# Optimization experiments

Hardware: AMD Instinct MI355X
Metric: run time of the kernel (lower is better)

The kernel has to match this reference:

```python
import jax, jax.numpy as jnp
import numpy as np

N_EMBD, N_HEAD, HEAD_DIM = 1024, 16, 64
N_EXPERTS, TOP_K, EXPERT_DIM = 8, 2, 2048
EPS = 1e-5


def rmsnorm(x):
    return x * jax.lax.rsqrt(jnp.mean(x * x, axis=-1, keepdims=True) + EPS)


def setup_inputs() -> dict:
    key = jax.random.key(0)
    ks = jax.random.split(key, 9)
    s = 0.02
    x = jax.random.normal(ks[0], (2, 2048, N_EMBD), dtype=jnp.float32)
    # weights stored [in, out] (torch Linear applies x @ W.T; we pre-transpose)
    wq = jax.random.normal(ks[1], (N_EMBD, N_EMBD), dtype=jnp.float32) * s
    wk = jax.random.normal(ks[2], (N_EMBD, N_EMBD), dtype=jnp.float32) * s
    wv = jax.random.normal(ks[3], (N_EMBD, N_EMBD), dtype=jnp.float32) * s
    wo = jax.random.normal(ks[4], (N_EMBD, N_EMBD), dtype=jnp.float32) * s
    router_w = jax.random.normal(ks[5], (N_EMBD, N_EXPERTS), dtype=jnp.float32) * s
    exp_fc1 = jax.random.normal(ks[6], (N_EXPERTS, N_EMBD, EXPERT_DIM), dtype=jnp.float32) * s
    exp_fc2 = jax.random.normal(ks[7], (N_EXPERTS, EXPERT_DIM, N_EMBD), dtype=jnp.float32) * s
    return {"x": x, "wq": wq, "wk": wk, "wv": wv, "wo": wo,
            "router_w": router_w, "exp_fc1": exp_fc1, "exp_fc2": exp_fc2}


def _attn(h, wq, wk, wv, wo):
    B, T, C = h.shape
    sc = 1.0 / np.sqrt(HEAD_DIM)
    q = (h @ wq).reshape(B, T, N_HEAD, HEAD_DIM)
    k = (h @ wk).reshape(B, T, N_HEAD, HEAD_DIM)
    v = (h @ wv).reshape(B, T, N_HEAD, HEAD_DIM)
    s = jnp.einsum('bqhd,bkhd->bhqk', q, k) * sc
    causal = jnp.triu(jnp.ones((T, T), dtype=bool), 1)
    s = jnp.where(causal, -jnp.inf, s)
    a = jax.nn.softmax(s, axis=-1)
    o = jnp.einsum('bhqk,bkhd->bqhd', a, v).reshape(B, T, C)
    return o @ wo


def _moe(h, router_w, exp_fc1, exp_fc2):
    B, T, D = h.shape
    xf = h.reshape(B * T, D)
    probs = jax.nn.softmax(xf @ router_w, axis=-1)          # [N, E]
    top_vals, top_idx = jax.lax.top_k(probs, TOP_K)          # [N, K]
    top_vals = top_vals / jnp.sum(top_vals, axis=-1, keepdims=True)
    # combine weight per (token, expert); top_k indices are distinct
    combine = jnp.sum(jax.nn.one_hot(top_idx, N_EXPERTS, dtype=xf.dtype)
                      * top_vals[..., None], axis=1)         # [N, E]
    h1 = jnp.square(jax.nn.relu(jnp.einsum('nd,edh->neh', xf, exp_fc1)))
    oe = jnp.einsum('neh,ehd->ned', h1, exp_fc2)             # [N, E, D]
    out = jnp.einsum('ned,ne->nd', oe, combine)
    return out.reshape(B, T, D)


def reference(x, wq, wk, wv, wo, router_w, exp_fc1, exp_fc2):
    x = x + _attn(rmsnorm(x), wq, wk, wv, wo)
    x = x + _moe(rmsnorm(x), router_w, exp_fc1, exp_fc2)
    return x
```

## Files before the change

kernel.cpp:

```cpp
#include <hip/hip_runtime.h>
#include <math.h>

#define NTOK 4096
#define DEMB 1024
#define TSEQ 2048
#define QKVS 3072
#define QKN  2048
#define EDIM 2048
#define NEXP 8

typedef unsigned short u16;
typedef unsigned int u32;
typedef __bf16 bf16_t;
typedef __bf16 bf16x8 __attribute__((ext_vector_type(8)));
typedef __bf16 bf16x4 __attribute__((ext_vector_type(4)));
typedef float f32x4 __attribute__((ext_vector_type(4)));

__device__ __forceinline__ f32x4 mfma16(bf16x8 a, bf16x8 b, f32x4 c) {
    return __builtin_amdgcn_mfma_f32_16x16x32_bf16(a, b, c, 0, 0, 0);
}
__device__ __forceinline__ void gll16(const void* g, void* l) {
    __builtin_amdgcn_global_load_lds((const __attribute__((address_space(1))) u32*)g,
                                     (__attribute__((address_space(3))) u32*)l, 16, 0, 0);
}
__device__ __forceinline__ u16 f2bf(float x) {
    union { __bf16 h; u16 u; } c; c.h = (__bf16)x; return c.u;
}

__global__ __launch_bounds__(256) void rmsnorm_split_k(const float* __restrict__ x,
                                                       bf16_t* __restrict__ hi,
                                                       bf16_t* __restrict__ lo) {
    const int row = blockIdx.x;
    const float4 v = ((const float4*)(x + (size_t)row * DEMB))[threadIdx.x];
    float ss = v.x*v.x + v.y*v.y + v.z*v.z + v.w*v.w;
    #pragma unroll
    for (int off = 32; off; off >>= 1) ss += __shfl_xor(ss, off);
    __shared__ float wsum[4];
    if ((threadIdx.x & 63) == 0) wsum[threadIdx.x >> 6] = ss;
    __syncthreads();
    const float r = rsqrtf((wsum[0]+wsum[1]+wsum[2]+wsum[3]) * (1.0f/DEMB) + 1e-5f);
    const float f[4] = {v.x*r, v.y*r, v.z*r, v.w*r};
    bf16x4 hv, lv;
    #pragma unroll
    for (int j = 0; j < 4; j++) {
        const __bf16 hb = (__bf16)f[j];
        hv[j] = hb;
        lv[j] = (__bf16)(f[j] - (float)hb);
    }
    ((bf16x4*)(hi + (size_t)row*DEMB))[threadIdx.x] = hv;
    ((bf16x4*)(lo + (size_t)row*DEMB))[threadIdx.x] = lv;
}

__global__ __launch_bounds__(256) void rmsnorm_bf_k(const float* __restrict__ x,
                                                    bf16_t* __restrict__ y) {
    const int row = blockIdx.x;
    const float4 v = ((const float4*)(x + (size_t)row * DEMB))[threadIdx.x];
    float ss = v.x*v.x + v.y*v.y + v.z*v.z + v.w*v.w;
    #pragma unroll
    for (int off = 32; off; off >>= 1) ss += __shfl_xor(ss, off);
    __shared__ float wsum[4];
    if ((threadIdx.x & 63) == 0) wsum[threadIdx.x >> 6] = ss;
    __syncthreads();
    const float r = rsqrtf((wsum[0]+wsum[1]+wsum[2]+wsum[3]) * (1.0f/DEMB) + 1e-5f);
    bf16x4 o;
    o[0] = (__bf16)(v.x*r); o[1] = (__bf16)(v.y*r);
    o[2] = (__bf16)(v.z*r); o[3] = (__bf16)(v.w*r);
    ((bf16x4*)(y + (size_t)row*DEMB))[threadIdx.x] = o;
}

__global__ __launch_bounds__(256) void transp_split_k(const float* __restrict__ w,
                                                      bf16_t* __restrict__ wth,
                                                      bf16_t* __restrict__ wtl,
                                                      int K, int M) {
    __shared__ float t[32][33];
    const int m0 = blockIdx.x*32, k0 = blockIdx.y*32;
    const int tx = threadIdx.x & 31, ty = threadIdx.x >> 5;
    #pragma unroll
    for (int i = 0; i < 32; i += 8) t[ty+i][tx] = w[(size_t)(k0+ty+i)*M + m0+tx];
    __syncthreads();
    #pragma unroll
    for (int i = 0; i < 32; i += 8) {
        const float f = t[tx][ty+i];
        const __bf16 hb = (__bf16)f;
        wth[(size_t)(m0+ty+i)*K + k0+tx] = hb;
        wtl[(size_t)(m0+ty+i)*K + k0+tx] = (__bf16)(f - (float)hb);
    }
}

__global__ __launch_bounds__(256) void transp_k(const float* __restrict__ w,
                                                bf16_t* __restrict__ wt,
                                                int K, int M) {
    __shared__ float t[32][33];
    const size_t eo = (size_t)blockIdx.z * K * M;
    w += eo; wt += eo;
    const int m0 = blockIdx.x*32, k0 = blockIdx.y*32;
    const int tx = threadIdx.x & 31, ty = threadIdx.x >> 5;
    #pragma unroll
    for (int i = 0; i < 32; i += 8) t[ty+i][tx] = w[(size_t)(k0+ty+i)*M + m0+tx];
    __syncthreads();
    #pragma unroll
    for (int i = 0; i < 32; i += 8) wt[(size_t)(m0+ty+i)*K + k0+tx] = (__bf16)t[tx][ty+i];
}

template<int EPI>
__global__ __launch_bounds__(256) void gemm_split(const bf16_t* __restrict__ Ah,
                                                  const bf16_t* __restrict__ Al,
                                                  const bf16_t* __restrict__ Bh,
                                                  const bf16_t* __restrict__ Bl,
                                                  const float* __restrict__ res,
                                                  float* __restrict__ C,
                                                  bf16_t* __restrict__ qkh,
                                                  bf16_t* __restrict__ qkl,
                                                  bf16_t* __restrict__ vth,
                                                  bf16_t* __restrict__ vtl,
                                                  int N, int K) {
    __shared__ u16 As[16384];
    __shared__ u16 Bs[16384];
    const int tid = threadIdx.x;
    const int lane = tid & 63, w = tid >> 6;
    const int lr = lane & 15, lg = lane >> 4;
    const int wm = w >> 1, wn = w & 1;
    const int nbx = gridDim.x;
    const int nwg = gridDim.x * gridDim.y;
    int flat = blockIdx.y * nbx + blockIdx.x;
    flat = (flat & 7) * (nwg >> 3) + (flat >> 3);
    const int m0 = (flat / nbx) * 128, n0 = (flat % nbx) * 128;

    const int srow = tid >> 3;
    const int sd   = (tid & 7) ^ (srow & 7);
    const int kofs = (sd & 3) * 8;
    const bf16_t* Asrc = (sd < 4) ? Ah : Al;
    const bf16_t* Bsrc = (sd < 4) ? Bh : Bl;
    const bf16_t* pa0 = Asrc + (size_t)(m0 + srow     ) * K + kofs;
    const bf16_t* pa1 = Asrc + (size_t)(m0 + srow + 32) * K + kofs;
    const bf16_t* pa2 = Asrc + (size_t)(m0 + srow + 64) * K + kofs;
    const bf16_t* pa3 = Asrc + (size_t)(m0 + srow + 96) * K + kofs;
    const bf16_t* pb0 = Bsrc + (size_t)(n0 + srow     ) * K + kofs;
    const bf16_t* pb1 = Bsrc + (size_t)(n0 + srow + 32) * K + kofs;
    const bf16_t* pb2 = Bsrc + (size_t)(n0 + srow + 64) * K + kofs;
    const bf16_t* pb3 = Bsrc + (size_t)(n0 + srow + 96) * K + kofs;
    char* dA = (char*)As + tid*16;
    char* dB = (char*)Bs + tid*16;
    const int ca = (lg ^ (lr & 7)) * 8;

    auto STG = [&](int bsel, int kk) {
        char* a_ = dA + bsel*16384;
        char* b_ = dB + bsel*16384;
        gll16(pa0 + kk, a_);          gll16(pa1 + kk, a_ + 4096);
        gll16(pa2 + kk, a_ + 8192);   gll16(pa3 + kk, a_ + 12288);
        gll16(pb0 + kk, b_);          gll16(pb1 + kk, b_ + 4096);
        gll16(pb2 + kk, b_ + 8192);   gll16(pb3 + kk, b_ + 12288);
    };

    STG(0, 0);
    asm volatile("s_waitcnt vmcnt(0)" ::: "memory");
    __syncthreads();
    f32x4 acc[4][4] = {};
    int cur = 0;
    for (int k0 = 0; k0 < K; k0 += 32) {
        if (k0 + 32 < K) STG(cur ^ 1, k0 + 32);
        const u16* Ab = As + cur*8192;
        const u16* Bb = Bs + cur*8192;
        bf16x8 ah[4], al[4], bh[4], bl[4];
        #pragma unroll
        for (int i = 0; i < 4; i++) {
            const int ao = (wm*64 + i*16 + lr)*64 + ca;
            const int bo = (wn*64 + i*16 + lr)*64 + ca;
            ah[i] = *(const bf16x8*)&Ab[ao];
            al[i] = *(const bf16x8*)&Ab[ao ^ 32];
            bh[i] = *(const bf16x8*)&Bb[bo];
            bl[i] = *(const bf16x8*)&Bb[bo ^ 32];
        }
        #pragma unroll
        for (int i = 0; i < 4; i++)
            #pragma unroll
            for (int j = 0; j < 4; j++) {
                acc[i][j] = mfma16(ah[i], bh[j], acc[i][j]);
                acc[i][j] = mfma16(ah[i], bl[j], acc[i][j]);
                acc[i][j] = mfma16(al[i], bh[j], acc[i][j]);
            }
        asm volatile("s_waitcnt vmcnt(0)" ::: "memory");
        __syncthreads();
        cur ^= 1;
    }
    #pragma unroll
    for (int i = 0; i < 4; i++) {
        #pragma unroll
        for (int j = 0; j < 4; j++) {
            const int row = m0 + wm*64 + i*16 + lg*4;
            const int col = n0 + wn*64 + j*16 + lr;
            const f32x4 v = acc[i][j];
            if (EPI == 1) {
                #pragma unroll
                for (int r = 0; r < 4; r++) {
                    const size_t o = (size_t)(row + r) * N + col;
                    C[o] = res[o] + v[r];
                }
            } else {
                if (col < QKN) {
                    const float sc = (col < DEMB) ? 0.125f : 1.0f;
                    #pragma unroll
                    for (int r = 0; r < 4; r++) {
                        const size_t o = (size_t)(row + r) * QKN + col;
                        const float f = v[r] * sc;
                        const __bf16 hb = (__bf16)f;
                        qkh[o] = hb;
                        qkl[o] = (__bf16)(f - (float)hb);
                    }
                } else {
                    const int d = col - QKN;
                    const int hh = d >> 6, dd = d & 63;
                    const int bb = row >> 11, t = row & 2047;
                    const size_t base = ((size_t)(bb*16 + hh)*64 + dd) * TSEQ + t;
                    #pragma unroll
                    for (int r = 0; r < 4; r++) {
                        const float f = v[r];
                        const __bf16 hb = (__bf16)f;
                        vth[base + r] = hb;
                        vtl[base + r] = (__bf16)(f - (float)hb);
                    }
                }
            }
        }
    }
}

template<int EPI, int GATHER>
__global__ __launch_bounds__(256) void gemm_moe(const bf16_t* __restrict__ A,
                                                const bf16_t* __restrict__ Ball,
                                                bf16_t* __restrict__ C,
                                                const int* __restrict__ rowmap,
                                                const int* __restrict__ counts,
                                                const int* __restrict__ offs,
                                                int N, int K) {
    const int e = blockIdx.z;
    const int cnt = counts[e];
    if ((int)blockIdx.y * 128 >= cnt) return;
    const int base = offs[e];
    const bf16_t* Bt = Ball + (size_t)e * N * K;
    __shared__ u16 As[8192];
    __shared__ u16 Bs[8192];
    const int tid = threadIdx.x;
    const int lane = tid & 63, w = tid >> 6;
    const int lr = lane & 15, lg = lane >> 4;
    const int wm = w >> 1, wn = w & 1;
    const int m0 = blockIdx.y * 128, n0 = blockIdx.x * 128;

    const int srp = tid >> 3;
    const int sd  = (tid & 7) ^ (srp & 7);
    const int smrow = 2*srp + (sd >> 2);
    const int kofs  = (sd & 3) * 8;
    const int l0 = min(m0 + smrow, cnt - 1), l1 = min(m0 + 64 + smrow, cnt - 1);
    const size_t r0 = GATHER ? (size_t)rowmap[base + l0] : (size_t)(base + l0);
    const size_t r1 = GATHER ? (size_t)rowmap[base + l1] : (size_t)(base + l1);
    const bf16_t* pa0 = A + r0 * K + kofs;
    const bf16_t* pa1 = A + r1 * K + kofs;
    const bf16_t* pb0 = Bt + (size_t)(n0 + smrow)      * K + kofs;
    const bf16_t* pb1 = Bt + (size_t)(n0 + 64 + smrow) * K + kofs;
    char* dA = (char*)As + tid*16;
    char* dB = (char*)Bs + tid*16;
    const int cs = (((lr & 1) << 2) + lg) ^ ((lr >> 1) & 7);

    auto STG = [&](int bsel, int kk) {
        char* a_ = dA + bsel*8192;
        char* b_ = dB + bsel*8192;
        gll16(pa0 + kk, a_); gll16(pa1 + kk, a_ + 4096);
        gll16(pb0 + kk, b_); gll16(pb1 + kk, b_ + 4096);
    };

    STG(0, 0);
    asm volatile("s_waitcnt vmcnt(0)" ::: "memory");
    __syncthreads();
    f32x4 acc[4][4] = {};
    int cur = 0;
    for (int k0 = 0; k0 < K; k0 += 32) {
        if (k0 + 32 < K) STG(cur ^ 1, k0 + 32);
        const u16* Ab = As + cur*4096;
        const u16* Bb = Bs + cur*4096;
        bf16x8 af[4], bfr[4];
        #pragma unroll
        for (int i = 0; i < 4; i++) {
            af[i]  = *(const bf16x8*)&Ab[(wm*32 + i*8 + (lr>>1))*64 + cs*8];
            bfr[i] = *(const bf16x8*)&Bb[(wn*32 + i*8 + (lr>>1))*64 + cs*8];
        }
        #pragma unroll
        for (int i = 0; i < 4; i++)
            #pragma unroll
            for (int j = 0; j < 4; j++)
                acc[i][j] = mfma16(af[i], bfr[j], acc[i][j]);
        asm volatile("s_waitcnt vmcnt(0)" ::: "memory");
        __syncthreads();
        cur ^= 1;
    }
    #pragma unroll
    for (int i = 0; i < 4; i++) {
        #pragma unroll
        for (int j = 0; j < 4; j++) {
            const int rowl = m0 + wm*64 + i*16 + lg*4;
            const int col  = n0 + wn*64 + j*16 + lr;
            const f32x4 v = acc[i][j];
            #pragma unroll
            for (int r = 0; r < 4; r++) {
                if (rowl + r < cnt) {
                    float xv = v[r];
                    if (EPI == 2) { xv = fmaxf(xv, 0.f); xv = xv * xv; }
                    C[(size_t)(base + rowl + r) * N + col] = (__bf16)xv;
                }
            }
        }
    }
}

__global__ __launch_bounds__(256) void attn_mfma(const bf16_t* __restrict__ qkh,
                                                 const bf16_t* __restrict__ qkl,
                                                 const bf16_t* __restrict__ vth,
                                                 const bf16_t* __restrict__ vtl,
                                                 bf16_t* __restrict__ aoh,
                                                 bf16_t* __restrict__ aol) {
    __shared__ u16 KsH[64*64];
    __shared__ u16 KsL[64*64];
    __shared__ u16 VtH[64*64];
    __shared__ u16 VtL[64*64];
    __shared__ u16 P_H[4*16*72];
    __shared__ u16 P_L[4*16*72];
    const int tid = threadIdx.x, lane = tid & 63, wv = tid >> 6;
    const int lr = lane & 15, lg = lane >> 4;
    const int L = blockIdx.x + blockIdx.y*16 + blockIdx.z*256;
    const int swz = (L & 7)*64 + (L >> 3);
    const int qa = swz & 15;
    const int h  = (swz >> 4) & 15;
    const int b  = swz >> 8;
    const int qb = 31 - qa;
    u16* plwH = P_H + wv * 16 * 72;
    u16* plwL = P_L + wv * 16 * 72;
    const int wq0A = qa*64 + wv*16;
    const int wq0B = qb*64 + wv*16;

    bf16x8 qAh[2], qAl[2], qBh[2], qBl[2];
    #pragma unroll
    for (int kf = 0; kf < 2; kf++) {
        const size_t qoA = (size_t)(b*TSEQ + wq0A + lr)*QKN + h*64 + kf*32 + lg*8;
        const size_t qoB = (size_t)(b*TSEQ + wq0B + lr)*QKN + h*64 + kf*32 + lg*8;
        qAh[kf] = *(const bf16x8*)(qkh + qoA);
        qAl[kf] = *(const bf16x8*)(qkl + qoA);
        qBh[kf] = *(const bf16x8*)(qkh + qoB);
        qBl[kf] = *(const bf16x8*)(qkl + qoB);
    }

    f32x4 ofA[4] = {}, ofB[4] = {};
    float mA = -1e30f, lA = 0.f, mB = -1e30f, lB = 0.f;

    const int skv = tid >> 3;
    const int pst = tid & 7;
    const int chs = pst ^ (skv & 7);
    const int bh = b*16 + h;
    const bf16_t* kh = qkh + 1024;
    const bf16_t* kl = qkl + 1024;
    const size_t vrow0 = (size_t)(bh*64 + skv)      * TSEQ;
    const size_t vrow1 = (size_t)(bh*64 + skv + 32) * TSEQ;

    auto step = [&](f32x4 (&of)[4], float& mrun, float& lrun,
                    const bf16x8 (&qfh)[2], const bf16x8 (&qfl)[2],
                    const int wq0, const bool diag, const int kvb) {
        f32x4 sf[4] = {};
        #pragma unroll
        for (int kf = 0; kf < 2; kf++)
            #pragma unroll
            for (int f = 0; f < 4; f++) {
                const int idx = (f*16 + lr)*64 + ((kf*32 + lg*8) ^ ((lr & 7) << 3));
                const bf16x8 ah = *(const bf16x8*)&KsH[idx];
                const bf16x8 al = *(const bf16x8*)&KsL[idx];
                sf[f] = mfma16(ah, qfh[kf], sf[f]);
                sf[f] = mfma16(ah, qfl[kf], sf[f]);
                sf[f] = mfma16(al, qfh[kf], sf[f]);
            }
        if (diag) {
            #pragma unroll
            for (int f = 0; f < 4; f++)
                #pragma unroll
                for (int r = 0; r < 4; r++)
                    if (kvb + f*16 + lg*4 + r > wq0 + lr) sf[f][r] = -1e30f;
        }
        float tm = -1e30f;
        #pragma unroll
        for (int f = 0; f < 4; f++)
            tm = fmaxf(tm, fmaxf(fmaxf(sf[f][0], sf[f][1]), fmaxf(sf[f][2], sf[f][3])));
        tm = fmaxf(tm, __shfl_xor(tm, 16));
        tm = fmaxf(tm, __shfl_xor(tm, 32));
        const float mnew = fmaxf(mrun, tm);
        const float fac = __expf(mrun - mnew);
        mrun = mnew;
        float ps = 0.f;
        #pragma unroll
        for (int f = 0; f < 4; f++) {
            float p[4];
            #pragma unroll
            for (int r = 0; r < 4; r++) { p[r] = __expf(sf[f][r] - mnew); ps += p[r]; }
            u16 hb4[4], lb4[4];
            #pragma unroll
            for (int r = 0; r < 4; r++) {
                const __bf16 hb = (__bf16)p[r];
                hb4[r] = f2bf(p[r]);
                lb4[r] = f2bf(p[r] - (float)hb);
            }
            u32* pwh = (u32*)&plwH[lr*72 + f*16 + lg*4];
            u32* pwl = (u32*)&plwL[lr*72 + f*16 + lg*4];
            pwh[0] = (u32)hb4[0] | ((u32)hb4[1] << 16);
            pwh[1] = (u32)hb4[2] | ((u32)hb4[3] << 16);
            pwl[0] = (u32)lb4[0] | ((u32)lb4[1] << 16);
            pwl[1] = (u32)lb4[2] | ((u32)lb4[3] << 16);
        }
        ps += __shfl_xor(ps, 16);
        ps += __shfl_xor(ps, 32);
        lrun = lrun*fac + ps;
        #pragma unroll
        for (int f2 = 0; f2 < 4; f2++)
            #pragma unroll
            for (int r = 0; r < 4; r++) of[f2][r] *= fac;
        #pragma unroll
        for (int hf = 0; hf < 2; hf++) {
            const bf16x8 pbh = *(const bf16x8*)&plwH[lr*72 + hf*32 + lg*8];
            const bf16x8 pbl = *(const bf16x8*)&plwL[lr*72 + hf*32 + lg*8];
            #pragma unroll
            for (int f2 = 0; f2 < 4; f2++) {
                const int vidx = (f2*16 + lr)*64 + (((hf*4 + lg) ^ (lr & 7)) << 3);
                const bf16x8 vah = *(const bf16x8*)&VtH[vidx];
                const bf16x8 val = *(const bf16x8*)&VtL[vidx];
                of[f2] = mfma16(vah, pbh, of[f2]);
                of[f2] = mfma16(vah, pbl, of[f2]);
                of[f2] = mfma16(val, pbh, of[f2]);
            }
        }
    };

    for (int kt = 0; kt <= qb; kt++) {
        __syncthreads();
        const size_t krow = (size_t)(b*TSEQ + kt*64 + skv)*QKN + h*64;
        gll16(kh + krow + chs*8,                     (char*)KsH + tid*16);
        gll16(kh + krow + (size_t)32*QKN + chs*8,    (char*)KsH + 4096 + tid*16);
        gll16(kl + krow + chs*8,                     (char*)KsL + tid*16);
        gll16(kl + krow + (size_t)32*QKN + chs*8,    (char*)KsL + 4096 + tid*16);
        gll16(vth + vrow0 + kt*64 + chs*8,           (char*)VtH + tid*16);
        gll16(vth + vrow1 + kt*64 + chs*8,           (char*)VtH + 4096 + tid*16);
        gll16(vtl + vrow0 + kt*64 + chs*8,           (char*)VtL + tid*16);
        gll16(vtl + vrow1 + kt*64 + chs*8,           (char*)VtL + 4096 + tid*16);
        __syncthreads();
        if (kt <= qa) step(ofA, mA, lA, qAh, qAl, wq0A, kt == qa, kt*64);
        step(ofB, mB, lB, qBh, qBl, wq0B, kt == qb, kt*64);
    }

    const float invA = 1.f / lA, invB = 1.f / lB;
    #pragma unroll
    for (int f2 = 0; f2 < 4; f2++) {
        u16 hb4[4], lb4[4];
        #pragma unroll
        for (int r = 0; r < 4; r++) {
            const float f = ofA[f2][r] * invA;
            const __bf16 hb = (__bf16)f;
            hb4[r] = f2bf(f);
            lb4[r] = f2bf(f - (float)hb);
        }
        u32* pwh = (u32*)&plwH[lr*72 + f2*16 + lg*4];
        u32* pwl = (u32*)&plwL[lr*72 + f2*16 + lg*4];
        pwh[0] = (u32)hb4[0] | ((u32)hb4[1] << 16);
        pwh[1] = (u32)hb4[2] | ((u32)hb4[3] << 16);
        pwl[0] = (u32)lb4[0] | ((u32)lb4[1] << 16);
        pwl[1] = (u32)lb4[2] | ((u32)lb4[3] << 16);
    }
    asm volatile("s_waitcnt lgkmcnt(0)" ::: "memory");
    __builtin_amdgcn_sched_barrier(0);
    #pragma unroll
    for (int pass = 0; pass < 2; pass++) {
        const int qlr = pass*8 + (lane >> 3);
        const int ch = (lane & 7) * 8;
        const bf16x8 oh = *(const bf16x8*)&plwH[qlr*72 + ch];
        const bf16x8 ol = *(const bf16x8*)&plwL[qlr*72 + ch];
        const size_t go = (size_t)(b*TSEQ + wq0A + qlr) * DEMB + h*64 + ch;
        *(bf16x8*)(aoh + go) = oh;
        *(bf16x8*)(aol + go) = ol;
    }
    asm volatile("s_waitcnt lgkmcnt(0)" ::: "memory");
    __builtin_amdgcn_sched_barrier(0);
    #pragma unroll
    for (int f2 = 0; f2 < 4; f2++) {
        u16 hb4[4], lb4[4];
        #pragma unroll
        for (int r = 0; r < 4; r++) {
            const float f = ofB[f2][r] * invB;
            const __bf16 hb = (__bf16)f;
            hb4[r] = f2bf(f);
            lb4[r] = f2bf(f - (float)hb);
        }
        u32* pwh = (u32*)&plwH[lr*72 + f2*16 + lg*4];
        u32* pwl = (u32*)&plwL[lr*72 + f2*16 + lg*4];
        pwh[0] = (u32)hb4[0] | ((u32)hb4[1] << 16);
        pwh[1] = (u32)hb4[2] | ((u32)hb4[3] << 16);
        pwl[0] = (u32)lb4[0] | ((u32)lb4[1] << 16);
        pwl[1] = (u32)lb4[2] | ((u32)lb4[3] << 16);
    }
    asm volatile("s_waitcnt lgkmcnt(0)" ::: "memory");
    __builtin_amdgcn_sched_barrier(0);
    #pragma unroll
    for (int pass = 0; pass < 2; pass++) {
        const int qlr = pass*8 + (lane >> 3);
        const int ch = (lane & 7) * 8;
        const bf16x8 oh = *(const bf16x8*)&plwH[qlr*72 + ch];
        const bf16x8 ol = *(const bf16x8*)&plwL[qlr*72 + ch];
        const size_t go = (size_t)(b*TSEQ + wq0B + qlr) * DEMB + h*64 + ch;
        *(bf16x8*)(aoh + go) = oh;
        *(bf16x8*)(aol + go) = ol;
    }
}

__global__ void zero8(int* c) { if (threadIdx.x < NEXP) c[threadIdx.x] = 0; }

__global__ __launch_bounds__(256) void router_k(const float* __restrict__ xout,
                                                const float* __restrict__ rw,
                                                int* __restrict__ idx,
                                                float* __restrict__ wts,
                                                int* __restrict__ pos,
                                                int* __restrict__ counts) {
    const int tok = blockIdx.x * 4 + (threadIdx.x >> 6);
    const int lane = threadIdx.x & 63;
    const float* xr = xout + (size_t)tok * DEMB;
    float ss = 0.f;
    float acc[NEXP];
    #pragma unroll
    for (int e = 0; e < NEXP; e++) acc[e] = 0.f;
    for (int kk = lane; kk < DEMB; kk += 64) {
        const float xv = xr[kk];
        ss += xv * xv;
        #pragma unroll
        for (int e = 0; e < NEXP; e++) acc[e] += xv * rw[kk*NEXP + e];
    }
    #pragma unroll
    for (int off = 32; off; off >>= 1) ss += __shfl_xor(ss, off);
    #pragma unroll
    for (int e = 0; e < NEXP; e++) {
        #pragma unroll
        for (int off = 32; off; off >>= 1) acc[e] += __shfl_xor(acc[e], off);
    }
    if (lane == 0) {
        const float r = rsqrtf(ss * (1.0f/DEMB) + 1e-5f);
        float v[NEXP];
        #pragma unroll
        for (int e = 0; e < NEXP; e++) v[e] = acc[e] * r;
        int b0 = 0; float v0 = v[0];
        #pragma unroll
        for (int e = 1; e < NEXP; e++) if (v[e] > v0) { v0 = v[e]; b0 = e; }
        int b1 = -1; float v1 = -1e30f;
        #pragma unroll
        for (int e = 0; e < NEXP; e++) if (e != b0 && v[e] > v1) { v1 = v[e]; b1 = e; }
        const float w0 = 1.f / (1.f + __expf(v1 - v0));
        idx[tok*2+0] = b0; idx[tok*2+1] = b1;
        wts[tok*2+0] = w0; wts[tok*2+1] = 1.f - w0;
        pos[tok*2+0] = atomicAdd(&counts[b0], 1);
        pos[tok*2+1] = atomicAdd(&counts[b1], 1);
    }
}

__global__ void offsets_k(const int* __restrict__ counts, int* __restrict__ offs) {
    if (threadIdx.x == 0) {
        int s = 0;
        for (int e = 0; e < NEXP; e++) { offs[e] = s; s += counts[e]; }
    }
}

__global__ __launch_bounds__(256) void buildmap_k(const int* __restrict__ idx,
                                                  const int* __restrict__ pos,
                                                  const int* __restrict__ offs,
                                                  int* __restrict__ rowmap,
                                                  int* __restrict__ rowpos) {
    const int n = blockIdx.x * 256 + threadIdx.x;
    #pragma unroll
    for (int s = 0; s < 2; s++) {
        const int e = idx[n*2+s];
        const int r = offs[e] + pos[n*2+s];
        rowmap[r] = n;
        rowpos[n*2+s] = r;
    }
}

__global__ __launch_bounds__(256) void combine_k(const bf16_t* __restrict__ oe,
                                                 const int* __restrict__ rowpos,
                                                 const float* __restrict__ wts,
                                                 float* __restrict__ out) {
    const int n = blockIdx.x;
    const int r0 = rowpos[n*2+0], r1 = rowpos[n*2+1];
    const float w0 = wts[n*2+0], w1 = wts[n*2+1];
    const int c = threadIdx.x * 4;
    const bf16x4 a  = *(const bf16x4*)(oe + (size_t)r0*DEMB + c);
    const bf16x4 b4 = *(const bf16x4*)(oe + (size_t)r1*DEMB + c);
    float4* op = (float4*)(out + (size_t)n*DEMB + c);
    float4 o = *op;
    o.x += w0*(float)a[0] + w1*(float)b4[0];
    o.y += w0*(float)a[1] + w1*(float)b4[1];
    o.z += w0*(float)a[2] + w1*(float)b4[2];
    o.w += w0*(float)a[3] + w1*(float)b4[3];
    *op = o;
}

extern "C" void kernel_launch(void* const* d_in, const int* in_sizes, int n_in,
                              void* d_out, int out_size, void* d_ws, size_t ws_size,
                              hipStream_t stream) {
    (void)in_sizes; (void)n_in; (void)out_size; (void)ws_size;
    const float* x   = (const float*)d_in[0];
    const float* wq  = (const float*)d_in[1];
    const float* wk  = (const float*)d_in[2];
    const float* wv  = (const float*)d_in[3];
    const float* wo  = (const float*)d_in[4];
    const float* rw  = (const float*)d_in[5];
    const float* fc1 = (const float*)d_in[6];
    const float* fc2 = (const float*)d_in[7];
    float* out = (float*)d_out;
    char* ws = (char*)d_ws;
    const size_t MB = 1024*1024;

    bf16_t* wqkv_h = (bf16_t*)(ws);
    bf16_t* wqkv_l = (bf16_t*)(ws + 6*MB);
    bf16_t* wo_h   = (bf16_t*)(ws + 12*MB);
    bf16_t* wo_l   = (bf16_t*)(ws + 14*MB);
    bf16_t* qk_h   = (bf16_t*)(ws + 16*MB);
    bf16_t* qk_l   = (bf16_t*)(ws + 32*MB);
    bf16_t* vt_h   = (bf16_t*)(ws + 48*MB);
    bf16_t* vt_l   = (bf16_t*)(ws + 56*MB);
    bf16_t* fc1_t  = (bf16_t*)(ws + 16*MB);
    bf16_t* fc2_t  = (bf16_t*)(ws + 48*MB);
    bf16_t* h_hi   = (bf16_t*)(ws + 64*MB);
    bf16_t* h_lo   = (bf16_t*)(ws + 72*MB);
    bf16_t* ao_h   = (bf16_t*)(ws + 64*MB);
    bf16_t* ao_l   = (bf16_t*)(ws + 72*MB);
    bf16_t* h      = (bf16_t*)(ws + 80*MB);
    bf16_t* h1     = (bf16_t*)(ws + 88*MB);
    bf16_t* oe     = (bf16_t*)(ws);
    char* meta = ws + 120*MB;
    int*   idx    = (int*)(meta);
    int*   pos    = (int*)(meta + 64*1024);
    int*   rowmap = (int*)(meta + 128*1024);
    int*   rowpos = (int*)(meta + 192*1024);
    float* wts    = (float*)(meta + 256*1024);
    int*   counts = (int*)(meta + 320*1024);
    int*   offs   = (int*)(meta + 320*1024 + 256);

    const dim3 blk(256);

    transp_split_k<<<dim3(32,32), blk, 0, stream>>>(wq, wqkv_h,               wqkv_l,               1024, 1024);
    transp_split_k<<<dim3(32,32), blk, 0, stream>>>(wk, wqkv_h + 1024*1024,   wqkv_l + 1024*1024,   1024, 1024);
    transp_split_k<<<dim3(32,32), blk, 0, stream>>>(wv, wqkv_h + 2*1024*1024, wqkv_l + 2*1024*1024, 1024, 1024);
    transp_split_k<<<dim3(32,32), blk, 0, stream>>>(wo, wo_h,                 wo_l,                 1024, 1024);
    rmsnorm_split_k<<<NTOK, blk, 0, stream>>>(x, h_hi, h_lo);
    gemm_split<3><<<dim3(QKVS/128, NTOK/128), blk, 0, stream>>>(
        h_hi, h_lo, wqkv_h, wqkv_l, nullptr, nullptr, qk_h, qk_l, vt_h, vt_l, QKVS, 1024);
    attn_mfma<<<dim3(16, 16, 2), blk, 0, stream>>>(qk_h, qk_l, vt_h, vt_l, ao_h, ao_l);
    gemm_split<1><<<dim3(DEMB/128, NTOK/128), blk, 0, stream>>>(
        ao_h, ao_l, wo_h, wo_l, x, out, nullptr, nullptr, nullptr, nullptr, DEMB, 1024);

    transp_k<<<dim3(64,32,8), blk, 0, stream>>>(fc1, fc1_t, 1024, 2048);
    transp_k<<<dim3(32,64,8), blk, 0, stream>>>(fc2, fc2_t, 2048, 1024);
    rmsnorm_bf_k<<<NTOK, blk, 0, stream>>>(out, h);
    zero8<<<1, 64, 0, stream>>>(counts);
    router_k<<<NTOK/4, blk, 0, stream>>>(out, rw, idx, wts, pos, counts);
    offsets_k<<<1, 64, 0, stream>>>(counts, offs);
    buildmap_k<<<NTOK/256, blk, 0, stream>>>(idx, pos, offs, rowmap, rowpos);
    gemm_moe<2,1><<<dim3(EDIM/128, 32, NEXP), blk, 0, stream>>>(
        h, fc1_t, h1, rowmap, counts, offs, EDIM, 1024);
    gemm_moe<3,0><<<dim3(DEMB/128, 32, NEXP), blk, 0, stream>>>(
        h1, fc2_t, oe, rowmap, counts, offs, DEMB, EDIM);
    combine_k<<<NTOK, blk, 0, stream>>>(oe, rowpos, wts, out);
}
```

Before: 526.0 us.

## Add 256x256-tile QKV GEMM and fuse MoE rmsnorm into router

Replaces the 128x128 QKV projection GEMM with a dedicated kernel using 256x256 tiles, 512 threads and 8 waves. The main loop is split into two half-phases that interleave global-to-LDS prefetch with MFMA work and raise wave priority around the MFMAs. Separately, the router kernel now keeps its token row in registers and writes the normalized bf16 activations itself, removing the standalone rmsnorm_bf launch and one extra read of the activations. The larger tile uses 128 KB of LDS and a big accumulator array, which risks low occupancy and register spilling. It also launches only 192 blocks, which may not fill all CUs.

```diff
diff --git a/kernel.cpp b/kernel.cpp
--- a/kernel.cpp
+++ b/kernel.cpp
@@ -49,23 +49,6 @@
     }
     ((bf16x4*)(hi + (size_t)row*DEMB))[threadIdx.x] = hv;
     ((bf16x4*)(lo + (size_t)row*DEMB))[threadIdx.x] = lv;
-}
-
-__global__ __launch_bounds__(256) void rmsnorm_bf_k(const float* __restrict__ x,
-                                                    bf16_t* __restrict__ y) {
-    const int row = blockIdx.x;
-    const float4 v = ((const float4*)(x + (size_t)row * DEMB))[threadIdx.x];
-    float ss = v.x*v.x + v.y*v.y + v.z*v.z + v.w*v.w;
-    #pragma unroll
-    for (int off = 32; off; off >>= 1) ss += __shfl_xor(ss, off);
-    __shared__ float wsum[4];
-    if ((threadIdx.x & 63) == 0) wsum[threadIdx.x >> 6] = ss;
-    __syncthreads();
-    const float r = rsqrtf((wsum[0]+wsum[1]+wsum[2]+wsum[3]) * (1.0f/DEMB) + 1e-5f);
-    bf16x4 o;
-    o[0] = (__bf16)(v.x*r); o[1] = (__bf16)(v.y*r);
-    o[2] = (__bf16)(v.z*r); o[3] = (__bf16)(v.w*r);
-    ((bf16x4*)(y + (size_t)row*DEMB))[threadIdx.x] = o;
 }
 
 __global__ __launch_bounds__(256) void transp_split_k(const float* __restrict__ w,
@@ -102,6 +85,151 @@
     for (int i = 0; i < 32; i += 8) wt[(size_t)(m0+ty+i)*K + k0+tx] = (__bf16)t[tx][ty+i];
 }
 
+__global__ __launch_bounds__(512) void gemm_qkv256(const bf16_t* __restrict__ Ah,
+                                                   const bf16_t* __restrict__ Al,
+                                                   const bf16_t* __restrict__ Bh,
+                                                   const bf16_t* __restrict__ Bl,
+                                                   bf16_t* __restrict__ qkh,
+                                                   bf16_t* __restrict__ qkl,
+                                                   bf16_t* __restrict__ vth,
+                                                   bf16_t* __restrict__ vtl) {
+    __shared__ u16 As[2*16384];
+    __shared__ u16 Bs[2*16384];
+    const int tid = threadIdx.x;
+    const int lane = tid & 63, w = tid >> 6;
+    const int lr = lane & 15, lg = lane >> 4;
+    const int wm = w >> 2, wn = w & 3;
+    int flat = blockIdx.y * 12 + blockIdx.x;
+    flat = (flat & 7) * 24 + (flat >> 3);
+    const int m0 = (flat / 12) * 256, n0 = (flat % 12) * 256;
+
+    const int srow = tid >> 3;
+    const int sd   = (tid & 7) ^ (srow & 7);
+    const int kofs = (sd & 3) * 8;
+    const bf16_t* Asrc = (sd < 4) ? Ah : Al;
+    const bf16_t* Bsrc = (sd < 4) ? Bh : Bl;
+    const bf16_t* pA0 = Asrc + (size_t)(m0 + srow      ) * 1024 + kofs;
+    const bf16_t* pA1 = Asrc + (size_t)(m0 + srow +  64) * 1024 + kofs;
+    const bf16_t* pA2 = Asrc + (size_t)(m0 + srow + 128) * 1024 + kofs;
+    const bf16_t* pA3 = Asrc + (size_t)(m0 + srow + 192) * 1024 + kofs;
+    const bf16_t* pB0 = Bsrc + (size_t)(n0 + srow      ) * 1024 + kofs;
+    const bf16_t* pB1 = Bsrc + (size_t)(n0 + srow +  64) * 1024 + kofs;
+    const bf16_t* pB2 = Bsrc + (size_t)(n0 + srow + 128) * 1024 + kofs;
+    const bf16_t* pB3 = Bsrc + (size_t)(n0 + srow + 192) * 1024 + kofs;
+    const int ca = (lg ^ (lr & 7)) * 8;
+
+#define STG_Q(u_, kn_, nb_) do { \
+    gll16(pA##u_ + (kn_), (char*)As + (nb_)*32768 + (u_)*8192 + tid*16); \
+    gll16(pB##u_ + (kn_), (char*)Bs + (nb_)*32768 + (u_)*8192 + tid*16); } while (0)
+
+    STG_Q(0, 0, 0); STG_Q(1, 0, 0); STG_Q(2, 0, 0); STG_Q(3, 0, 0);
+    asm volatile("s_waitcnt vmcnt(0)" ::: "memory");
+    __builtin_amdgcn_sched_barrier(0);
+    __syncthreads();
+
+    f32x4 acc[8][4] = {};
+    int cur = 0;
+    for (int t = 0; t < 32; t++) {
+        const u16* Ab = As + cur*16384;
+        const u16* Bb = Bs + cur*16384;
+        const int nb = cur ^ 1;
+        const int kn = (t + 1) * 32;
+        const bool more = (t < 31);
+
+        bf16x8 bh[4], bl[4];
+        #pragma unroll
+        for (int j = 0; j < 4; j++) {
+            const int bo = (wn*64 + j*16 + lr)*64 + ca;
+            bh[j] = *(const bf16x8*)&Bb[bo];
+            bl[j] = *(const bf16x8*)&Bb[bo ^ 32];
+        }
+        {
+            bf16x8 ah[4], al[4];
+            #pragma unroll
+            for (int i = 0; i < 4; i++) {
+                const int ao = (wm*128 + i*16 + lr)*64 + ca;
+                ah[i] = *(const bf16x8*)&Ab[ao];
+                al[i] = *(const bf16x8*)&Ab[ao ^ 32];
+            }
+            if (more) { STG_Q(0, kn, nb); STG_Q(1, kn, nb); }
+            __builtin_amdgcn_s_barrier();
+            asm volatile("s_waitcnt lgkmcnt(0)" ::: "memory");
+            __builtin_amdgcn_sched_barrier(0);
+            __builtin_amdgcn_s_setprio(1);
+            #pragma unroll
+            for (int i = 0; i < 4; i++)
+                #pragma unroll
+                for (int j = 0; j < 4; j++) {
+                    acc[i][j] = mfma16(ah[i], bh[j], acc[i][j]);
+                    acc[i][j] = mfma16(ah[i], bl[j], acc[i][j]);
+                    acc[i][j] = mfma16(al[i], bh[j], acc[i][j]);
+                }
+            __builtin_amdgcn_s_setprio(0);
+            __builtin_amdgcn_s_barrier();
+        }
+        {
+            bf16x8 ah[4], al[4];
+            #pragma unroll
+            for (int i = 0; i < 4; i++) {
+                const int ao = (wm*128 + 64 + i*16 + lr)*64 + ca;
+                ah[i] = *(const bf16x8*)&Ab[ao];
+                al[i] = *(const bf16x8*)&Ab[ao ^ 32];
+            }
+            if (more) { STG_Q(2, kn, nb); STG_Q(3, kn, nb); }
+            __builtin_amdgcn_s_barrier();
+            asm volatile("s_waitcnt lgkmcnt(0)" ::: "memory");
+            __builtin_amdgcn_sched_barrier(0);
+            __builtin_amdgcn_s_setprio(1);
+            #pragma unroll
+            for (int i = 0; i < 4; i++)
+                #pragma unroll
+                for (int j = 0; j < 4; j++) {
+                    acc[4+i][j] = mfma16(ah[i], bh[j], acc[4+i][j]);
+                    acc[4+i][j] = mfma16(ah[i], bl[j], acc[4+i][j]);
+                    acc[4+i][j] = mfma16(al[i], bh[j], acc[4+i][j]);
+                }
+            __builtin_amdgcn_s_setprio(0);
+            asm volatile("s_waitcnt vmcnt(0)" ::: "memory");
+            __builtin_amdgcn_sched_barrier(0);
+            __builtin_amdgcn_s_barrier();
+        }
+        cur ^= 1;
+    }
+#undef STG_Q
+    #pragma unroll
+    for (int i = 0; i < 8; i++) {
+        #pragma unroll
+        for (int j = 0; j < 4; j++) {
+            const int row = m0 + wm*128 + i*16 + lg*4;
+            const int col = n0 + wn*64 + j*16 + lr;
+            const f32x4 v = acc[i][j];
+            if (col < QKN) {
+                const float sc = (col < DEMB) ? 0.125f : 1.0f;
+                #pragma unroll
+                for (int r = 0; r < 4; r++) {
+                    const size_t o = (size_t)(row + r) * QKN + col;
+                    const float f = v[r] * sc;
+                    const __bf16 hb = (__bf16)f;
+                    qkh[o] = hb;
+                    qkl[o] = (__bf16)(f - (float)hb);
+                }
+            } else {
+                const int d = col - QKN;
+                const int hh = d >> 6, dd = d & 63;
+                const int bb = row >> 11, tt = row & 2047;
+                const size_t base = ((size_t)(bb*16 + hh)*64 + dd) * TSEQ + tt;
+                #pragma unroll
+                for (int r = 0; r < 4; r++) {
+                    const float f = v[r];
+                    const __bf16 hb = (__bf16)f;
+                    vth[base + r] = hb;
+                    vtl[base + r] = (__bf16)(f - (float)hb);
+                }
+            }
+        }
+    }
+}
+
 template<int EPI>
 __global__ __launch_bounds__(256) void gemm_split(const bf16_t* __restrict__ Ah,
                                                   const bf16_t* __restrict__ Al,
@@ -109,10 +237,6 @@
                                                   const bf16_t* __restrict__ Bl,
                                                   const float* __restrict__ res,
                                                   float* __restrict__ C,
-                                                  bf16_t* __restrict__ qkh,
-                                                  bf16_t* __restrict__ qkl,
-                                                  bf16_t* __restrict__ vth,
-                                                  bf16_t* __restrict__ vtl,
                                                   int N, int K) {
     __shared__ u16 As[16384];
     __shared__ u16 Bs[16384];
@@ -190,36 +314,10 @@
             const int row = m0 + wm*64 + i*16 + lg*4;
             const int col = n0 + wn*64 + j*16 + lr;
             const f32x4 v = acc[i][j];
-            if (EPI == 1) {
-                #pragma unroll
-                for (int r = 0; r < 4; r++) {
-                    const size_t o = (size_t)(row + r) * N + col;
-                    C[o] = res[o] + v[r];
-                }
-            } else {
-                if (col < QKN) {
-                    const float sc = (col < DEMB) ? 0.125f : 1.0f;
-                    #pragma unroll
-                    for (int r = 0; r < 4; r++) {
-                        const size_t o = (size_t)(row + r) * QKN + col;
-                        const float f = v[r] * sc;
-                        const __bf16 hb = (__bf16)f;
-                        qkh[o] = hb;
-                        qkl[o] = (__bf16)(f - (float)hb);
-                    }
-                } else {
-                    const int d = col - QKN;
-                    const int hh = d >> 6, dd = d & 63;
-                    const int bb = row >> 11, t = row & 2047;
-                    const size_t base = ((size_t)(bb*16 + hh)*64 + dd) * TSEQ + t;
-                    #pragma unroll
-                    for (int r = 0; r < 4; r++) {
-                        const float f = v[r];
-                        const __bf16 hb = (__bf16)f;
-                        vth[base + r] = hb;
-                        vtl[base + r] = (__bf16)(f - (float)hb);
-                    }
-                }
+            #pragma unroll
+            for (int r = 0; r < 4; r++) {
+                const size_t o = (size_t)(row + r) * N + col;
+                C[o] = res[o] + v[r];
             }
         }
     }
@@ -399,9 +497,9 @@
             u16 hb4[4], lb4[4];
             #pragma unroll
             for (int r = 0; r < 4; r++) {
-                const __bf16 hb = (__bf16)p[r];
+                const __bf16 hbv = (__bf16)p[r];
                 hb4[r] = f2bf(p[r]);
-                lb4[r] = f2bf(p[r] - (float)hb);
+                lb4[r] = f2bf(p[r] - (float)hbv);
             }
             u32* pwh = (u32*)&plwH[lr*72 + f*16 + lg*4];
             u32* pwl = (u32*)&plwL[lr*72 + f*16 + lg*4];
@@ -456,9 +554,9 @@
         #pragma unroll
         for (int r = 0; r < 4; r++) {
             const float f = ofA[f2][r] * invA;
-            const __bf16 hb = (__bf16)f;
+            const __bf16 hbv = (__bf16)f;
             hb4[r] = f2bf(f);
-            lb4[r] = f2bf(f - (float)hb);
+            lb4[r] = f2bf(f - (float)hbv);
         }
         u32* pwh = (u32*)&plwH[lr*72 + f2*16 + lg*4];
         u32* pwl = (u32*)&plwL[lr*72 + f2*16 + lg*4];
@@ -487,9 +585,9 @@
         #pragma unroll
         for (int r = 0; r < 4; r++) {
             const float f = ofB[f2][r] * invB;
-            const __bf16 hb = (__bf16)f;
+            const __bf16 hbv = (__bf16)f;
             hb4[r] = f2bf(f);
-            lb4[r] = f2bf(f - (float)hb);
+            lb4[r] = f2bf(f - (float)hbv);
         }
         u32* pwh = (u32*)&plwH[lr*72 + f2*16 + lg*4];
         u32* pwl = (u32*)&plwL[lr*72 + f2*16 + lg*4];
@@ -516,6 +614,7 @@
 
 __global__ __launch_bounds__(256) void router_k(const float* __restrict__ xout,
                                                 const float* __restrict__ rw,
+                                                bf16_t* __restrict__ h,
                                                 int* __restrict__ idx,
                                                 float* __restrict__ wts,
                                                 int* __restrict__ pos,
@@ -523,12 +622,16 @@
     const int tok = blockIdx.x * 4 + (threadIdx.x >> 6);
     const int lane = threadIdx.x & 63;
     const float* xr = xout + (size_t)tok * DEMB;
+    float xv16[16];
     float ss = 0.f;
     float acc[NEXP];
     #pragma unroll
     for (int e = 0; e < NEXP; e++) acc[e] = 0.f;
-    for (int kk = lane; kk < DEMB; kk += 64) {
+    #pragma unroll
+    for (int i = 0; i < 16; i++) {
+        const int kk = lane + i*64;
         const float xv = xr[kk];
+        xv16[i] = xv;
         ss += xv * xv;
         #pragma unroll
         for (int e = 0; e < NEXP; e++) acc[e] += xv * rw[kk*NEXP + e];
@@ -540,8 +643,11 @@
         #pragma unroll
         for (int off = 32; off; off >>= 1) acc[e] += __shfl_xor(acc[e], off);
     }
+    const float r = rsqrtf(ss * (1.0f/DEMB) + 1e-5f);
+    #pragma unroll
+    for (int i = 0; i < 16; i++)
+        h[(size_t)tok*DEMB + lane + i*64] = (__bf16)(xv16[i] * r);
     if (lane == 0) {
-        const float r = rsqrtf(ss * (1.0f/DEMB) + 1e-5f);
         float v[NEXP];
         #pragma unroll
         for (int e = 0; e < NEXP; e++) v[e] = acc[e] * r;
@@ -649,17 +755,16 @@
     transp_split_k<<<dim3(32,32), blk, 0, stream>>>(wv, wqkv_h + 2*1024*1024, wqkv_l + 2*1024*1024, 1024, 1024);
     transp_split_k<<<dim3(32,32), blk, 0, stream>>>(wo, wo_h,                 wo_l,                 1024, 1024);
     rmsnorm_split_k<<<NTOK, blk, 0, stream>>>(x, h_hi, h_lo);
-    gemm_split<3><<<dim3(QKVS/128, NTOK/128), blk, 0, stream>>>(
-        h_hi, h_lo, wqkv_h, wqkv_l, nullptr, nullptr, qk_h, qk_l, vt_h, vt_l, QKVS, 1024);
+    gemm_qkv256<<<dim3(12, 16), dim3(512), 0, stream>>>(
+        h_hi, h_lo, wqkv_h, wqkv_l, qk_h, qk_l, vt_h, vt_l);
     attn_mfma<<<dim3(16, 16, 2), blk, 0, stream>>>(qk_h, qk_l, vt_h, vt_l, ao_h, ao_l);
     gemm_split<1><<<dim3(DEMB/128, NTOK/128), blk, 0, stream>>>(
-        ao_h, ao_l, wo_h, wo_l, x, out, nullptr, nullptr, nullptr, nullptr, DEMB, 1024);
+        ao_h, ao_l, wo_h, wo_l, x, out, DEMB, 1024);
 
     transp_k<<<dim3(64,32,8), blk, 0, stream>>>(fc1, fc1_t, 1024, 2048);
     transp_k<<<dim3(32,64,8), blk, 0, stream>>>(fc2, fc2_t, 2048, 1024);
-    rmsnorm_bf_k<<<NTOK, blk, 0, stream>>>(out, h);
     zero8<<<1, 64, 0, stream>>>(counts);
-    router_k<<<NTOK/4, blk, 0, stream>>>(out, rw, idx, wts, pos, counts);
+    router_k<<<NTOK/4, blk, 0, stream>>>(out, rw, h, idx, wts, pos, counts);
     offsets_k<<<1, 64, 0, stream>>>(counts, offs);
     buildmap_k<<<NTOK/256, blk, 0, stream>>>(idx, pos, offs, rowmap, rowpos);
     gemm_moe<2,1><<<dim3(EDIM/128, 32, NEXP), blk, 0, stream>>>(
```

Measured after the change: 507.9 us. 3.4% less time.
